# Optimization experiments

Hardware: AMD Instinct MI355X
Metric: run time of the kernel (lower is better)

Reference implementation:

```python
import jax, jax.numpy as jnp
import numpy as np

B, P, ENC = 64, 49, 1280
T, V, E, H, A = 25, 10000, 512, 1024, 512


def setup_inputs() -> dict:
    key = jax.random.key(0)
    ks = jax.random.split(key, 20)
    s = 0.02
    return {
        "encoder_out": jax.random.normal(ks[0], (B, P, ENC), jnp.float32),
        "captions": jax.random.randint(ks[1], (B, T), 0, V, jnp.int32),
        "embed": jax.random.normal(ks[2], (V, E), jnp.float32) * s,
        "W_eatt": jax.random.normal(ks[3], (A, ENC), jnp.float32) * s,
        "b_eatt": jnp.zeros((A,), jnp.float32),
        "W_datt": jax.random.normal(ks[4], (A, H), jnp.float32) * s,
        "b_datt": jnp.zeros((A,), jnp.float32),
        "W_fatt": jax.random.normal(ks[5], (1, A), jnp.float32) * s,
        "b_fatt": jnp.zeros((1,), jnp.float32),
        "W_ih": jax.random.normal(ks[6], (4 * H, E + ENC), jnp.float32) * s,
        "b_ih": jnp.zeros((4 * H,), jnp.float32),
        "W_hh": jax.random.normal(ks[7], (4 * H, H), jnp.float32) * s,
        "b_hh": jnp.zeros((4 * H,), jnp.float32),
        "W_h0": jax.random.normal(ks[8], (H, ENC), jnp.float32) * s,
        "b_h0": jnp.zeros((H,), jnp.float32),
        "W_c0": jax.random.normal(ks[9], (H, ENC), jnp.float32) * s,
        "b_c0": jnp.zeros((H,), jnp.float32),
        "W_out": jax.random.normal(ks[10], (V, H), jnp.float32) * s,
        "b_out": jnp.zeros((V,), jnp.float32),
    }


def reference(encoder_out, captions, embed, W_eatt, b_eatt, W_datt, b_datt,
              W_fatt, b_fatt, W_ih, b_ih, W_hh, b_hh, W_h0, b_h0, W_c0, b_c0,
              W_out, b_out):
    emb = embed[captions]                       # [B,T,E]
    mean_enc = encoder_out.mean(axis=1)         # [B,ENC]
    h0 = mean_enc @ W_h0.T + b_h0               # [B,H]
    c0 = mean_enc @ W_c0.T + b_c0
    # encoder-side attention projection is step-invariant; hoist out of loop
    att1 = encoder_out @ W_eatt.T + b_eatt      # [B,P,A]
    nH = h0.shape[-1]

    def step(carry, x_t):
        h, c = carry
        att2 = h @ W_datt.T + b_datt                          # [B,A]
        e = (jax.nn.relu(att1 + att2[:, None, :]) @ W_fatt.T + b_fatt)[..., 0]  # [B,P]
        alpha = jax.nn.softmax(e, axis=1)
        ctx = jnp.einsum('bp,bpe->be', alpha, encoder_out)    # [B,ENC]
        gin = jnp.concatenate([x_t, ctx], axis=1)             # [B,E+ENC]
        gates = gin @ W_ih.T + b_ih + h @ W_hh.T + b_hh       # [B,4H]
        i, f, g, o = jnp.split(gates, 4, axis=1)
        c_new = jax.nn.sigmoid(f) * c + jax.nn.sigmoid(i) * jnp.tanh(g)
        h_new = jax.nn.sigmoid(o) * jnp.tanh(c_new)
        preds = h_new @ W_out.T + b_out                       # dropout in eval mode = identity
        return (h_new, c_new), preds

    xs = jnp.swapaxes(emb[:, :-1, :], 0, 1)     # [T-1,B,E]
    _, preds = jax.lax.scan(step, (h0, c0), xs)
    return jnp.swapaxes(preds, 0, 1)            # [B,T-1,V]
```

## Files before the change

### kernel.cpp

```cpp
#include <hip/hip_runtime.h>
#include <hip/hip_bf16.h>

typedef float  v4f __attribute__((ext_vector_type(4)));
typedef short  v8s __attribute__((ext_vector_type(8)));
typedef int    v4i __attribute__((ext_vector_type(4)));

#define DEV static __device__ __forceinline__

DEV float bf2f(unsigned short u) {
    union { unsigned int i; float f; } x; x.i = ((unsigned int)u) << 16; return x.f;
}
DEV unsigned short f2bf(float f) {
    union { float f; unsigned int i; } x; x.f = f;
    unsigned int r = x.i + 0x7fff + ((x.i >> 16) & 1);
    return (unsigned short)(r >> 16);
}
DEV float sigm(float x) { return 1.f / (1.f + __expf(-x)); }

DEV v4i pack8(const float* f) {
    v4i o;
#pragma unroll
    for (int q = 0; q < 4; ++q)
        ((unsigned int*)&o)[q] = (unsigned int)f2bf(f[2 * q]) |
                                 ((unsigned int)f2bf(f[2 * q + 1]) << 16);
    return o;
}
DEV float lo16(unsigned int x) { union { unsigned int i; float f; } u; u.i = x << 16; return u.f; }
DEV float hi16(unsigned int x) { union { unsigned int i; float f; } u; u.i = x & 0xffff0000u; return u.f; }

__global__ __launch_bounds__(256) void uber_init(
    const float* __restrict__ Wih, const float* __restrict__ Whh,
    const float* __restrict__ bih, const float* __restrict__ bhh,
    const float* __restrict__ WoutF, const float* __restrict__ WeattF,
    const float* __restrict__ WdattF, const float* __restrict__ Wh0F,
    const float* __restrict__ Wc0F, const float* __restrict__ enc,
    const int* __restrict__ caps, const float* __restrict__ embed,
    unsigned short* __restrict__ Wz, unsigned short* __restrict__ Woutb,
    unsigned short* __restrict__ Weattb, unsigned short* __restrict__ Wdattb,
    unsigned short* __restrict__ Wh0b, unsigned short* __restrict__ Wc0b,
    unsigned short* __restrict__ encb, unsigned short* __restrict__ embb,
    unsigned short* __restrict__ meanb, float* __restrict__ bz)
{
    const int i = (blockIdx.x * 256 + threadIdx.x) * 8;
    float f[8];
    if (i < 11534336) {
        int n = i / 2816, k = i - n * 2816;
        const float* src = (k < 1792) ? &Wih[n * 1792 + k] : &Whh[n * 1024 + (k - 1792)];
        *(v4f*)&f[0] = *(const v4f*)src; *(v4f*)&f[4] = *(const v4f*)(src + 4);
        *(v4i*)&Wz[i] = pack8(f);
    } else if (i < 21774336) {
        int j = i - 11534336;
        *(v4f*)&f[0] = *(const v4f*)&WoutF[j]; *(v4f*)&f[4] = *(const v4f*)&WoutF[j + 4];
        *(v4i*)&Woutb[j] = pack8(f);
    } else if (i < 22429696) {
        int j = i - 21774336;
        *(v4f*)&f[0] = *(const v4f*)&WeattF[j]; *(v4f*)&f[4] = *(const v4f*)&WeattF[j + 4];
        *(v4i*)&Weattb[j] = pack8(f);
    } else if (i < 22953984) {
        int j = i - 22429696;
        *(v4f*)&f[0] = *(const v4f*)&WdattF[j]; *(v4f*)&f[4] = *(const v4f*)&WdattF[j + 4];
        *(v4i*)&Wdattb[j] = pack8(f);
    } else if (i < 24264704) {
        int j = i - 22953984;
        *(v4f*)&f[0] = *(const v4f*)&Wh0F[j]; *(v4f*)&f[4] = *(const v4f*)&Wh0F[j + 4];
        *(v4i*)&Wh0b[j] = pack8(f);
    } else if (i < 25575424) {
        int j = i - 24264704;
        *(v4f*)&f[0] = *(const v4f*)&Wc0F[j]; *(v4f*)&f[4] = *(const v4f*)&Wc0F[j + 4];
        *(v4i*)&Wc0b[j] = pack8(f);
    } else if (i < 29589504) {
        int j = i - 25575424;
        *(v4f*)&f[0] = *(const v4f*)&enc[j]; *(v4f*)&f[4] = *(const v4f*)&enc[j + 4];
        *(v4i*)&encb[j] = pack8(f);
    } else if (i < 30375936) {
        int j = i - 29589504;
        int b = j / 12288, r = j - b * 12288, t = r / 512, e = r - t * 512;
        const float* src = &embed[caps[b * 25 + t] * 512 + e];
        *(v4f*)&f[0] = *(const v4f*)src; *(v4f*)&f[4] = *(const v4f*)(src + 4);
        *(v4i*)&embb[j] = pack8(f);
    } else if (i < 30457856) {
        int j = i - 30375936;
        int b = j / 1280, c = j - b * 1280;
#pragma unroll
        for (int q = 0; q < 8; ++q) f[q] = 0.f;
        for (int p = 0; p < 49; ++p) {
            const float* src = &enc[(b * 49 + p) * 1280 + c];
            v4f a = *(const v4f*)src, bq = *(const v4f*)(src + 4);
#pragma unroll
            for (int q = 0; q < 4; ++q) { f[q] += a[q]; f[q + 4] += bq[q]; }
        }
#pragma unroll
        for (int q = 0; q < 8; ++q) f[q] *= (1.f / 49.f);
        *(v4i*)&meanb[j] = pack8(f);
    } else if (i < 30461952) {
        int j = i - 30457856;
#pragma unroll
        for (int q = 0; q < 8; ++q) f[q] = bih[j + q] + bhh[j + q];
        *(v4f*)&bz[j] = *(v4f*)&f[0]; *(v4f*)&bz[j + 4] = *(v4f*)&f[4];
    }
}

template <int OUT_BF16>
__global__ __launch_bounds__(256) void gemm64_bn16(
    const unsigned short* __restrict__ Ag, int lda,
    const unsigned short* __restrict__ Bg, int K,
    const float* __restrict__ bias, void* __restrict__ Cg, int ldc)
{
    __shared__ unsigned short lA[64 * 264];
    __shared__ unsigned short lB[16 * 264];
    const int tid = threadIdx.x, lane = tid & 63, w = tid >> 6;
    const int nb = blockIdx.x * 16;
    const int rA = tid >> 5, cA = (tid & 31) * 8;
    v4f acc = {0.f, 0.f, 0.f, 0.f};
    v4i ra[8], rb[2];
#pragma unroll
    for (int i = 0; i < 8; ++i)
        ra[i] = *(const v4i*)&Ag[(rA + i * 8) * lda + cA];
#pragma unroll
    for (int i = 0; i < 2; ++i)
        rb[i] = *(const v4i*)&Bg[(nb + rA + i * 8) * K + cA];
    for (int kt = 0; kt < K; kt += 256) {
#pragma unroll
        for (int i = 0; i < 8; ++i) *(v4i*)&lA[(rA + i * 8) * 264 + cA] = ra[i];
#pragma unroll
        for (int i = 0; i < 2; ++i) *(v4i*)&lB[(rA + i * 8) * 264 + cA] = rb[i];
        __syncthreads();
        if (kt + 256 < K) {
#pragma unroll
            for (int i = 0; i < 8; ++i)
                ra[i] = *(const v4i*)&Ag[(rA + i * 8) * lda + kt + 256 + cA];
#pragma unroll
            for (int i = 0; i < 2; ++i)
                rb[i] = *(const v4i*)&Bg[(nb + rA + i * 8) * K + kt + 256 + cA];
        }
#pragma unroll
        for (int ks = 0; ks < 8; ++ks) {
            v8s a = *(const v8s*)&lA[(w * 16 + (lane & 15)) * 264 + ks * 32 + (lane >> 4) * 8];
            v8s b = *(const v8s*)&lB[(lane & 15) * 264 + ks * 32 + (lane >> 4) * 8];
            acc = __builtin_amdgcn_mfma_f32_16x16x32_bf16(a, b, acc, 0, 0, 0);
        }
        __syncthreads();
    }
    const int n = nb + (lane & 15);
    const float bs = bias[n];
#pragma unroll
    for (int r = 0; r < 4; ++r) {
        int m = w * 16 + (lane >> 4) * 4 + r;
        float v = acc[r] + bs;
        if (OUT_BF16) ((unsigned short*)Cg)[m * ldc + n] = f2bf(v);
        else          ((float*)Cg)[m * ldc + n] = v;
    }
}

__global__ __launch_bounds__(256) void gemm_att1_k(
    const unsigned short* __restrict__ Aenc, const unsigned short* __restrict__ Bw,
    const float* __restrict__ bias, unsigned short* __restrict__ Cout)
{
    __shared__ unsigned short lA[64 * 136];
    __shared__ unsigned short lB[64 * 136];
    const int tid = threadIdx.x, lane = tid & 63, w = tid >> 6;
    const int mb = blockIdx.y * 64, nb = blockIdx.x * 64;
    const int rT = tid >> 4, cT = (tid & 15) * 8;
    v4f acc[4];
#pragma unroll
    for (int f = 0; f < 4; ++f) acc[f] = (v4f){0.f, 0.f, 0.f, 0.f};
    v4i ra[4], rb[4];
#pragma unroll
    for (int i = 0; i < 4; ++i) {
        ra[i] = *(const v4i*)&Aenc[(mb + rT + i * 16) * 1280 + cT];
        rb[i] = *(const v4i*)&Bw[(nb + rT + i * 16) * 1280 + cT];
    }
    for (int kt = 0; kt < 1280; kt += 128) {
#pragma unroll
        for (int i = 0; i < 4; ++i) {
            *(v4i*)&lA[(rT + i * 16) * 136 + cT] = ra[i];
            *(v4i*)&lB[(rT + i * 16) * 136 + cT] = rb[i];
        }
        __syncthreads();
        if (kt + 128 < 1280) {
#pragma unroll
            for (int i = 0; i < 4; ++i) {
                ra[i] = *(const v4i*)&Aenc[(mb + rT + i * 16) * 1280 + kt + 128 + cT];
                rb[i] = *(const v4i*)&Bw[(nb + rT + i * 16) * 1280 + kt + 128 + cT];
            }
        }
#pragma unroll
        for (int ks = 0; ks < 4; ++ks) {
            v8s a = *(const v8s*)&lA[(w * 16 + (lane & 15)) * 136 + ks * 32 + (lane >> 4) * 8];
#pragma unroll
            for (int f = 0; f < 4; ++f) {
                v8s b = *(const v8s*)&lB[(f * 16 + (lane & 15)) * 136 + ks * 32 + (lane >> 4) * 8];
                acc[f] = __builtin_amdgcn_mfma_f32_16x16x32_bf16(a, b, acc[f], 0, 0, 0);
            }
        }
        __syncthreads();
    }
#pragma unroll
    for (int f = 0; f < 4; ++f) {
        int n = nb + f * 16 + (lane & 15);
        float bs = bias[n];
#pragma unroll
        for (int r = 0; r < 4; ++r) {
            int m = mb + w * 16 + (lane >> 4) * 4 + r;
            Cout[m * 512 + n] = f2bf(acc[f][r] + bs);
        }
    }
}

__global__ __launch_bounds__(256) void attn_ctx_k(
    const float* __restrict__ att2, const unsigned short* __restrict__ att1b,
    const float* __restrict__ Wfatt, const float* __restrict__ bfatt,
    const unsigned short* __restrict__ encb, const unsigned short* __restrict__ embb,
    unsigned short* __restrict__ z, int tstep)
{
    __shared__ float a2[512];
    __shared__ float wf[512];
    __shared__ float es[64];
    __shared__ float alpha[64];
    const int tid = threadIdx.x, lane = tid & 63, w = tid >> 6;
    const int b = blockIdx.x;
    a2[tid]       = att2[b * 512 + tid];
    a2[tid + 256] = att2[b * 512 + tid + 256];
    wf[tid]       = Wfatt[tid];
    wf[tid + 256] = Wfatt[tid + 256];
    __syncthreads();
    for (int p = w; p < 49; p += 4) {
        v4i u = *(const v4i*)&att1b[(b * 49 + p) * 512 + lane * 8];
        v4f c0 = *(const v4f*)&a2[lane * 8], c1 = *(const v4f*)&a2[lane * 8 + 4];
        v4f w0 = *(const v4f*)&wf[lane * 8], w1 = *(const v4f*)&wf[lane * 8 + 4];
        float s = 0.f;
#pragma unroll
        for (int q = 0; q < 4; ++q) {
            unsigned int x = ((unsigned int*)&u)[q];
            float vlo = lo16(x), vhi = hi16(x);
            float clo = (q < 2) ? c0[q * 2] : c1[q * 2 - 4];
            float chi = (q < 2) ? c0[q * 2 + 1] : c1[q * 2 - 3];
            float wlo = (q < 2) ? w0[q * 2] : w1[q * 2 - 4];
            float whi = (q < 2) ? w0[q * 2 + 1] : w1[q * 2 - 3];
            s += fmaxf(vlo + clo, 0.f) * wlo;
            s += fmaxf(vhi + chi, 0.f) * whi;
        }
#pragma unroll
        for (int off = 32; off > 0; off >>= 1) s += __shfl_xor(s, off);
        if (lane == 0) es[p] = s + bfatt[0];
    }
    __syncthreads();
    if (w == 0) {
        float v = (lane < 49) ? es[lane] : -1e30f;
        float m = v;
#pragma unroll
        for (int off = 32; off > 0; off >>= 1) m = fmaxf(m, __shfl_xor(m, off));
        float e = (lane < 49) ? __expf(v - m) : 0.f;
        float s = e;
#pragma unroll
        for (int off = 32; off > 0; off >>= 1) s += __shfl_xor(s, off);
        if (lane < 49) alpha[lane] = e / s;
    }
    __syncthreads();
    if (tid < 160) {
        const int jb = tid * 8;
        float acc[8];
#pragma unroll
        for (int q = 0; q < 8; ++q) acc[q] = 0.f;
        for (int p = 0; p < 49; ++p) {
            v4i u = *(const v4i*)&encb[(b * 49 + p) * 1280 + jb];
            float al = alpha[p];
#pragma unroll
            for (int q = 0; q < 4; ++q) {
                unsigned int x = ((unsigned int*)&u)[q];
                acc[2 * q]     += al * lo16(x);
                acc[2 * q + 1] += al * hi16(x);
            }
        }
        *(v4i*)&z[b * 2816 + 512 + jb] = pack8(acc);
    }
    if (tid < 64)
        *(v4i*)&z[b * 2816 + tid * 8] = *(const v4i*)&embb[(b * 24 + tstep) * 512 + tid * 8];
}

__global__ __launch_bounds__(256) void gates_lstm_k(
    const unsigned short* __restrict__ z, const unsigned short* __restrict__ Wz,
    const float* __restrict__ bz, float* __restrict__ cst,
    unsigned short* __restrict__ zh, unsigned short* __restrict__ HallT)
{
    __shared__ unsigned short lA[64 * 264];
    __shared__ unsigned short lB[16 * 264];
    __shared__ float gbuf[64 * 20];
    const int tid = threadIdx.x, lane = tid & 63, w = tid >> 6;
    const int hb = blockIdx.x * 4;
    const int rT = tid >> 5, cT = (tid & 31) * 8;
    const int gate = rT & 3, hco = rT >> 2;
    const int growB = (gate * 1024 + hb + hco) * 2816;
    const int growB2 = (((rT + 8) & 3) * 1024 + hb + ((rT + 8) >> 2)) * 2816;
    v4f acc = {0.f, 0.f, 0.f, 0.f};
    v4i ra[8], rb[2];
#pragma unroll
    for (int i = 0; i < 8; ++i)
        ra[i] = *(const v4i*)&z[(rT + i * 8) * 2816 + cT];
    rb[0] = *(const v4i*)&Wz[growB + cT];
    rb[1] = *(const v4i*)&Wz[growB2 + cT];
    for (int kt = 0; kt < 2816; kt += 256) {
#pragma unroll
        for (int i = 0; i < 8; ++i) *(v4i*)&lA[(rT + i * 8) * 264 + cT] = ra[i];
        *(v4i*)&lB[rT * 264 + cT] = rb[0];
        *(v4i*)&lB[(rT + 8) * 264 + cT] = rb[1];
        __syncthreads();
        if (kt + 256 < 2816) {
#pragma unroll
            for (int i = 0; i < 8; ++i)
                ra[i] = *(const v4i*)&z[(rT + i * 8) * 2816 + kt + 256 + cT];
            rb[0] = *(const v4i*)&Wz[growB + kt + 256 + cT];
            rb[1] = *(const v4i*)&Wz[growB2 + kt + 256 + cT];
        }
#pragma unroll
        for (int ks = 0; ks < 8; ++ks) {
            v8s a = *(const v8s*)&lA[(w * 16 + (lane & 15)) * 264 + ks * 32 + (lane >> 4) * 8];
            v8s b = *(const v8s*)&lB[(lane & 15) * 264 + ks * 32 + (lane >> 4) * 8];
            acc = __builtin_amdgcn_mfma_f32_16x16x32_bf16(a, b, acc, 0, 0, 0);
        }
        __syncthreads();
    }
#pragma unroll
    for (int r = 0; r < 4; ++r) {
        int m = w * 16 + (lane >> 4) * 4 + r;
        int n = lane & 15;
        gbuf[m * 20 + n] = acc[r];
    }
    __syncthreads();
    const int b = tid >> 2, hc2 = tid & 3, hidx = hb + hc2;
    float gi = gbuf[b * 20 + hc2 * 4 + 0] + bz[hidx];
    float gf = gbuf[b * 20 + hc2 * 4 + 1] + bz[1024 + hidx];
    float gg = gbuf[b * 20 + hc2 * 4 + 2] + bz[2048 + hidx];
    float go = gbuf[b * 20 + hc2 * 4 + 3] + bz[3072 + hidx];
    float cn = sigm(gf) * cst[b * 1024 + hidx] + sigm(gi) * tanhf(gg);
    float hn = sigm(go) * tanhf(cn);
    cst[b * 1024 + hidx] = cn;
    unsigned short hb16 = f2bf(hn);
    zh[b * 2816 + hidx] = hb16;
    HallT[b * 1024 + hidx] = hb16;
}

__global__ __launch_bounds__(256) void preds_k(
    const unsigned short* __restrict__ Hall, const unsigned short* __restrict__ Wout,
    const float* __restrict__ bout, float* __restrict__ out)
{
    __shared__ unsigned short lA[128 * 72];
    __shared__ unsigned short lB[128 * 72];
    const int tid = threadIdx.x, lane = tid & 63, w = tid >> 6;
    const int mb = blockIdx.y * 128, nb = blockIdx.x * 128;
    const int rT = tid >> 3, cT = (tid & 7) * 8;
    int nB = nb + rT; if (nB > 9999) nB = 9999;
    v4f acc[2][8];
#pragma unroll
    for (int i = 0; i < 2; ++i)
#pragma unroll
        for (int f = 0; f < 8; ++f) acc[i][f] = (v4f){0.f, 0.f, 0.f, 0.f};
    v4i ra[4], rb[4];
#pragma unroll
    for (int i = 0; i < 4; ++i) {
        ra[i] = *(const v4i*)&Hall[(mb + rT + i * 32) * 1024 + cT];
        int n2 = nb + rT + i * 32; if (n2 > 9999) n2 = 9999;
        rb[i] = *(const v4i*)&Wout[n2 * 1024 + cT];
    }
    for (int kt = 0; kt < 1024; kt += 64) {
#pragma unroll
        for (int i = 0; i < 4; ++i) {
            *(v4i*)&lA[(rT + i * 32) * 72 + cT] = ra[i];
            *(v4i*)&lB[(rT + i * 32) * 72 + cT] = rb[i];
        }
        __syncthreads();
        if (kt + 64 < 1024) {
#pragma unroll
            for (int i = 0; i < 4; ++i) {
                ra[i] = *(const v4i*)&Hall[(mb + rT + i * 32) * 1024 + kt + 64 + cT];
                int n2 = nb + rT + i * 32; if (n2 > 9999) n2 = 9999;
                rb[i] = *(const v4i*)&Wout[n2 * 1024 + kt + 64 + cT];
            }
        }
#pragma unroll
        for (int ks = 0; ks < 2; ++ks) {
            int ko = ks * 32 + (lane >> 4) * 8;
            v8s a0 = *(const v8s*)&lA[(w * 32 + (lane & 15)) * 72 + ko];
            v8s a1 = *(const v8s*)&lA[(w * 32 + 16 + (lane & 15)) * 72 + ko];
#pragma unroll
            for (int f = 0; f < 8; ++f) {
                v8s b = *(const v8s*)&lB[(f * 16 + (lane & 15)) * 72 + ko];
                acc[0][f] = __builtin_amdgcn_mfma_f32_16x16x32_bf16(a0, b, acc[0][f], 0, 0, 0);
                acc[1][f] = __builtin_amdgcn_mfma_f32_16x16x32_bf16(a1, b, acc[1][f], 0, 0, 0);
            }
        }
        __syncthreads();
    }
#pragma unroll
    for (int f = 0; f < 8; ++f) {
        int n = nb + f * 16 + (lane & 15);
        if (n < 10000) {
            float bs = bout[n];
#pragma unroll
            for (int i = 0; i < 2; ++i)
#pragma unroll
                for (int r = 0; r < 4; ++r) {
                    int m = mb + w * 32 + i * 16 + (lane >> 4) * 4 + r;
                    int tt = m >> 6, bb = m & 63;
                    out[(bb * 24 + tt) * 10000 + n] = acc[i][f][r] + bs;
                }
        }
    }
}

extern "C" void kernel_launch(void* const* d_in, const int* in_sizes, int n_in,
                              void* d_out, int out_size, void* d_ws, size_t ws_size,
                              hipStream_t stream)
{
    const float* enc   = (const float*)d_in[0];
    const int*   caps  = (const int*)d_in[1];
    const float* embed = (const float*)d_in[2];
    const float* Weatt = (const float*)d_in[3];
    const float* beatt = (const float*)d_in[4];
    const float* Wdatt = (const float*)d_in[5];
    const float* bdatt = (const float*)d_in[6];
    const float* Wfatt = (const float*)d_in[7];
    const float* bfatt = (const float*)d_in[8];
    const float* Wih   = (const float*)d_in[9];
    const float* bih   = (const float*)d_in[10];
    const float* Whh   = (const float*)d_in[11];
    const float* bhh   = (const float*)d_in[12];
    const float* Wh0   = (const float*)d_in[13];
    const float* bh0   = (const float*)d_in[14];
    const float* Wc0   = (const float*)d_in[15];
    const float* bc0   = (const float*)d_in[16];
    const float* WoutF = (const float*)d_in[17];
    const float* bout  = (const float*)d_in[18];
    float* out = (float*)d_out;

    char* ws = (char*)d_ws;
    size_t off = 0;
    auto carve = [&](size_t bytes) -> void* {
        void* p = ws + off; off += (bytes + 255) & ~(size_t)255; return p;
    };
    unsigned short* Wzb    = (unsigned short*)carve(11534336ull * 2);
    unsigned short* Woutb  = (unsigned short*)carve(10240000ull * 2);
    unsigned short* Weattb = (unsigned short*)carve(655360ull * 2);
    unsigned short* Wdattb = (unsigned short*)carve(524288ull * 2);
    unsigned short* Wh0b   = (unsigned short*)carve(1310720ull * 2);
    unsigned short* Wc0b   = (unsigned short*)carve(1310720ull * 2);
    unsigned short* encb   = (unsigned short*)carve(4014080ull * 2);
    unsigned short* embb   = (unsigned short*)carve(786432ull * 2);
    unsigned short* meanb  = (unsigned short*)carve(81920ull * 2);
    unsigned short* att1b  = (unsigned short*)carve(1605632ull * 2);
    unsigned short* Hallb  = (unsigned short*)carve(1572864ull * 2);
    unsigned short* zb     = (unsigned short*)carve(180224ull * 2);
    float* bz   = (float*)carve(4096ull * 4);
    float* att2 = (float*)carve(32768ull * 4);
    float* cst  = (float*)carve(65536ull * 4);

    uber_init<<<14874, 256, 0, stream>>>(Wih, Whh, bih, bhh, WoutF, Weatt, Wdatt,
        Wh0, Wc0, enc, caps, embed, Wzb, Woutb, Weattb, Wdattb, Wh0b, Wc0b,
        encb, embb, meanb, bz);

    gemm64_bn16<1><<<64, 256, 0, stream>>>(meanb, 1280, Wh0b, 1280, bh0, zb + 1792, 2816);
    gemm64_bn16<0><<<64, 256, 0, stream>>>(meanb, 1280, Wc0b, 1280, bc0, cst, 1024);

    gemm_att1_k<<<dim3(8, 49), 256, 0, stream>>>(encb, Weattb, beatt, att1b);

    for (int t = 0; t < 24; ++t) {
        gemm64_bn16<0><<<32, 256, 0, stream>>>(zb + 1792, 2816, Wdattb, 1024, bdatt, att2, 512);
        attn_ctx_k<<<64, 256, 0, stream>>>(att2, att1b, Wfatt, bfatt, encb, embb, zb, t);
        gates_lstm_k<<<256, 256, 0, stream>>>(zb, Wzb, bz, cst, zb + 1792,
                                              Hallb + (size_t)t * 64 * 1024);
    }

    preds_k<<<dim3(79, 12), 256, 0, stream>>>(Hallb, Woutb, bout, out);
}
```

Baseline: 1.133 ms.

## Fuse recurrent loop into persistent kernel with global atomic barriers

Replaces the 72 per-timestep kernel launches (att2 GEMM, attention/context, gates+LSTM) with one persistent 256-block kernel that runs all 24 steps, separating the phases with a software grid barrier built on an atomic counter. The hidden state moves to a separate hnew buffer that is copied into z during the attention phase. The output projection kernel also gets a 1D grid with an XCD-aware block-to-tile mapping to improve L2 locality. This removes launch overhead and inter-kernel gaps, but it depends on all 256 blocks being co-resident and adds barrier spin cost.

Result: slower. 4.130 ms (+264.4%).

```diff
diff --git a/kernel.cpp b/kernel.cpp
--- a/kernel.cpp
+++ b/kernel.cpp
@@ -27,6 +27,18 @@
 }
 DEV float lo16(unsigned int x) { union { unsigned int i; float f; } u; u.i = x << 16; return u.f; }
 DEV float hi16(unsigned int x) { union { unsigned int i; float f; } u; u.i = x & 0xffff0000u; return u.f; }
+
+DEV void gbar(int* cnt, int target) {
+    __syncthreads();
+    if (threadIdx.x == 0) {
+        __threadfence();
+        __hip_atomic_fetch_add(cnt, 1, __ATOMIC_RELEASE, __HIP_MEMORY_SCOPE_AGENT);
+        while (__hip_atomic_load(cnt, __ATOMIC_ACQUIRE, __HIP_MEMORY_SCOPE_AGENT) < target)
+            __builtin_amdgcn_s_sleep(2);
+        __threadfence();
+    }
+    __syncthreads();
+}
 
 __global__ __launch_bounds__(256) void uber_init(
     const float* __restrict__ Wih, const float* __restrict__ Whh,
@@ -207,149 +219,215 @@
     }
 }
 
-__global__ __launch_bounds__(256) void attn_ctx_k(
-    const float* __restrict__ att2, const unsigned short* __restrict__ att1b,
-    const float* __restrict__ Wfatt, const float* __restrict__ bfatt,
-    const unsigned short* __restrict__ encb, const unsigned short* __restrict__ embb,
-    unsigned short* __restrict__ z, int tstep)
+struct SmemGemm {
+    unsigned short lA[64 * 264];
+    unsigned short lB[16 * 264];
+    float gbuf[64 * 20];
+};
+struct SmemAttn {
+    float a2[512];
+    float wf[512];
+    float es[64];
+    float alpha[64];
+};
+union LoopSmem { SmemGemm g; SmemAttn a; };
+
+__global__ __launch_bounds__(256, 1) void loop_k(
+    float* __restrict__ att2, unsigned short* __restrict__ zb,
+    const unsigned short* __restrict__ Wdattb, const float* __restrict__ bdatt,
+    const unsigned short* __restrict__ att1b, const float* __restrict__ Wfatt,
+    const float* __restrict__ bfatt, const unsigned short* __restrict__ encb,
+    const unsigned short* __restrict__ embb, const unsigned short* __restrict__ Wzb,
+    const float* __restrict__ bz, float* __restrict__ cst,
+    unsigned short* __restrict__ Hallb, unsigned short* __restrict__ hnewb,
+    int* __restrict__ barcnt)
 {
-    __shared__ float a2[512];
-    __shared__ float wf[512];
-    __shared__ float es[64];
-    __shared__ float alpha[64];
+    __shared__ LoopSmem sm;
     const int tid = threadIdx.x, lane = tid & 63, w = tid >> 6;
-    const int b = blockIdx.x;
-    a2[tid]       = att2[b * 512 + tid];
-    a2[tid + 256] = att2[b * 512 + tid + 256];
-    wf[tid]       = Wfatt[tid];
-    wf[tid + 256] = Wfatt[tid + 256];
-    __syncthreads();
-    for (int p = w; p < 49; p += 4) {
-        v4i u = *(const v4i*)&att1b[(b * 49 + p) * 512 + lane * 8];
-        v4f c0 = *(const v4f*)&a2[lane * 8], c1 = *(const v4f*)&a2[lane * 8 + 4];
-        v4f w0 = *(const v4f*)&wf[lane * 8], w1 = *(const v4f*)&wf[lane * 8 + 4];
-        float s = 0.f;
-#pragma unroll
-        for (int q = 0; q < 4; ++q) {
-            unsigned int x = ((unsigned int*)&u)[q];
-            float vlo = lo16(x), vhi = hi16(x);
-            float clo = (q < 2) ? c0[q * 2] : c1[q * 2 - 4];
-            float chi = (q < 2) ? c0[q * 2 + 1] : c1[q * 2 - 3];
-            float wlo = (q < 2) ? w0[q * 2] : w1[q * 2 - 4];
-            float whi = (q < 2) ? w0[q * 2 + 1] : w1[q * 2 - 3];
-            s += fmaxf(vlo + clo, 0.f) * wlo;
-            s += fmaxf(vhi + chi, 0.f) * whi;
-        }
-#pragma unroll
-        for (int off = 32; off > 0; off >>= 1) s += __shfl_xor(s, off);
-        if (lane == 0) es[p] = s + bfatt[0];
-    }
-    __syncthreads();
-    if (w == 0) {
-        float v = (lane < 49) ? es[lane] : -1e30f;
-        float m = v;
-#pragma unroll
-        for (int off = 32; off > 0; off >>= 1) m = fmaxf(m, __shfl_xor(m, off));
-        float e = (lane < 49) ? __expf(v - m) : 0.f;
-        float s = e;
-#pragma unroll
-        for (int off = 32; off > 0; off >>= 1) s += __shfl_xor(s, off);
-        if (lane < 49) alpha[lane] = e / s;
-    }
-    __syncthreads();
-    if (tid < 160) {
-        const int jb = tid * 8;
-        float acc[8];
-#pragma unroll
-        for (int q = 0; q < 8; ++q) acc[q] = 0.f;
-        for (int p = 0; p < 49; ++p) {
-            v4i u = *(const v4i*)&encb[(b * 49 + p) * 1280 + jb];
-            float al = alpha[p];
-#pragma unroll
-            for (int q = 0; q < 4; ++q) {
-                unsigned int x = ((unsigned int*)&u)[q];
-                acc[2 * q]     += al * lo16(x);
-                acc[2 * q + 1] += al * hi16(x);
-            }
-        }
-        *(v4i*)&z[b * 2816 + 512 + jb] = pack8(acc);
-    }
-    if (tid < 64)
-        *(v4i*)&z[b * 2816 + tid * 8] = *(const v4i*)&embb[(b * 24 + tstep) * 512 + tid * 8];
-}
-
-__global__ __launch_bounds__(256) void gates_lstm_k(
-    const unsigned short* __restrict__ z, const unsigned short* __restrict__ Wz,
-    const float* __restrict__ bz, float* __restrict__ cst,
-    unsigned short* __restrict__ zh, unsigned short* __restrict__ HallT)
-{
-    __shared__ unsigned short lA[64 * 264];
-    __shared__ unsigned short lB[16 * 264];
-    __shared__ float gbuf[64 * 20];
-    const int tid = threadIdx.x, lane = tid & 63, w = tid >> 6;
-    const int hb = blockIdx.x * 4;
-    const int rT = tid >> 5, cT = (tid & 31) * 8;
-    const int gate = rT & 3, hco = rT >> 2;
-    const int growB = (gate * 1024 + hb + hco) * 2816;
-    const int growB2 = (((rT + 8) & 3) * 1024 + hb + ((rT + 8) >> 2)) * 2816;
-    v4f acc = {0.f, 0.f, 0.f, 0.f};
-    v4i ra[8], rb[2];
-#pragma unroll
-    for (int i = 0; i < 8; ++i)
-        ra[i] = *(const v4i*)&z[(rT + i * 8) * 2816 + cT];
-    rb[0] = *(const v4i*)&Wz[growB + cT];
-    rb[1] = *(const v4i*)&Wz[growB2 + cT];
-    for (int kt = 0; kt < 2816; kt += 256) {
-#pragma unroll
-        for (int i = 0; i < 8; ++i) *(v4i*)&lA[(rT + i * 8) * 264 + cT] = ra[i];
-        *(v4i*)&lB[rT * 264 + cT] = rb[0];
-        *(v4i*)&lB[(rT + 8) * 264 + cT] = rb[1];
-        __syncthreads();
-        if (kt + 256 < 2816) {
+    const int bid = blockIdx.x;
+    int btarget = 0;
+
+    for (int t = 0; t < 24; ++t) {
+        if (bid < 32) {
+            const int nb = bid * 16;
+            const int rA = tid >> 5, cA = (tid & 31) * 8;
+            v4f acc = {0.f, 0.f, 0.f, 0.f};
+            v4i ra[8], rb[2];
 #pragma unroll
             for (int i = 0; i < 8; ++i)
-                ra[i] = *(const v4i*)&z[(rT + i * 8) * 2816 + kt + 256 + cT];
-            rb[0] = *(const v4i*)&Wz[growB + kt + 256 + cT];
-            rb[1] = *(const v4i*)&Wz[growB2 + kt + 256 + cT];
-        }
-#pragma unroll
-        for (int ks = 0; ks < 8; ++ks) {
-            v8s a = *(const v8s*)&lA[(w * 16 + (lane & 15)) * 264 + ks * 32 + (lane >> 4) * 8];
-            v8s b = *(const v8s*)&lB[(lane & 15) * 264 + ks * 32 + (lane >> 4) * 8];
-            acc = __builtin_amdgcn_mfma_f32_16x16x32_bf16(a, b, acc, 0, 0, 0);
-        }
-        __syncthreads();
-    }
-#pragma unroll
-    for (int r = 0; r < 4; ++r) {
-        int m = w * 16 + (lane >> 4) * 4 + r;
-        int n = lane & 15;
-        gbuf[m * 20 + n] = acc[r];
-    }
-    __syncthreads();
-    const int b = tid >> 2, hc2 = tid & 3, hidx = hb + hc2;
-    float gi = gbuf[b * 20 + hc2 * 4 + 0] + bz[hidx];
-    float gf = gbuf[b * 20 + hc2 * 4 + 1] + bz[1024 + hidx];
-    float gg = gbuf[b * 20 + hc2 * 4 + 2] + bz[2048 + hidx];
-    float go = gbuf[b * 20 + hc2 * 4 + 3] + bz[3072 + hidx];
-    float cn = sigm(gf) * cst[b * 1024 + hidx] + sigm(gi) * tanhf(gg);
-    float hn = sigm(go) * tanhf(cn);
-    cst[b * 1024 + hidx] = cn;
-    unsigned short hb16 = f2bf(hn);
-    zh[b * 2816 + hidx] = hb16;
-    HallT[b * 1024 + hidx] = hb16;
+                ra[i] = *(const v4i*)&hnewb[(rA + i * 8) * 1024 + cA];
+#pragma unroll
+            for (int i = 0; i < 2; ++i)
+                rb[i] = *(const v4i*)&Wdattb[(nb + rA + i * 8) * 1024 + cA];
+            for (int kt = 0; kt < 1024; kt += 256) {
+#pragma unroll
+                for (int i = 0; i < 8; ++i) *(v4i*)&sm.g.lA[(rA + i * 8) * 264 + cA] = ra[i];
+#pragma unroll
+                for (int i = 0; i < 2; ++i) *(v4i*)&sm.g.lB[(rA + i * 8) * 264 + cA] = rb[i];
+                __syncthreads();
+                if (kt + 256 < 1024) {
+#pragma unroll
+                    for (int i = 0; i < 8; ++i)
+                        ra[i] = *(const v4i*)&hnewb[(rA + i * 8) * 1024 + kt + 256 + cA];
+#pragma unroll
+                    for (int i = 0; i < 2; ++i)
+                        rb[i] = *(const v4i*)&Wdattb[(nb + rA + i * 8) * 1024 + kt + 256 + cA];
+                }
+#pragma unroll
+                for (int ks = 0; ks < 8; ++ks) {
+                    v8s a = *(const v8s*)&sm.g.lA[(w * 16 + (lane & 15)) * 264 + ks * 32 + (lane >> 4) * 8];
+                    v8s b = *(const v8s*)&sm.g.lB[(lane & 15) * 264 + ks * 32 + (lane >> 4) * 8];
+                    acc = __builtin_amdgcn_mfma_f32_16x16x32_bf16(a, b, acc, 0, 0, 0);
+                }
+                __syncthreads();
+            }
+            const int n = nb + (lane & 15);
+            const float bs = bdatt[n];
+#pragma unroll
+            for (int r = 0; r < 4; ++r) {
+                int m = w * 16 + (lane >> 4) * 4 + r;
+                att2[m * 512 + n] = acc[r] + bs;
+            }
+        }
+        btarget += 256; gbar(barcnt, btarget);
+
+        if (bid < 64) {
+            const int b = bid;
+            float* a2 = sm.a.a2; float* wf = sm.a.wf;
+            float* es = sm.a.es; float* alpha = sm.a.alpha;
+            a2[tid]       = att2[b * 512 + tid];
+            a2[tid + 256] = att2[b * 512 + tid + 256];
+            wf[tid]       = Wfatt[tid];
+            wf[tid + 256] = Wfatt[tid + 256];
+            __syncthreads();
+            for (int p = w; p < 49; p += 4) {
+                v4i u = *(const v4i*)&att1b[(b * 49 + p) * 512 + lane * 8];
+                v4f c0 = *(const v4f*)&a2[lane * 8], c1 = *(const v4f*)&a2[lane * 8 + 4];
+                v4f w0 = *(const v4f*)&wf[lane * 8], w1 = *(const v4f*)&wf[lane * 8 + 4];
+                float s = 0.f;
+#pragma unroll
+                for (int q = 0; q < 4; ++q) {
+                    unsigned int x = ((unsigned int*)&u)[q];
+                    float vlo = lo16(x), vhi = hi16(x);
+                    float clo = (q < 2) ? c0[q * 2] : c1[q * 2 - 4];
+                    float chi = (q < 2) ? c0[q * 2 + 1] : c1[q * 2 - 3];
+                    float wlo = (q < 2) ? w0[q * 2] : w1[q * 2 - 4];
+                    float whi = (q < 2) ? w0[q * 2 + 1] : w1[q * 2 - 3];
+                    s += fmaxf(vlo + clo, 0.f) * wlo;
+                    s += fmaxf(vhi + chi, 0.f) * whi;
+                }
+#pragma unroll
+                for (int off = 32; off > 0; off >>= 1) s += __shfl_xor(s, off);
+                if (lane == 0) es[p] = s + bfatt[0];
+            }
+            __syncthreads();
+            if (w == 0) {
+                float v = (lane < 49) ? es[lane] : -1e30f;
+                float m = v;
+#pragma unroll
+                for (int off = 32; off > 0; off >>= 1) m = fmaxf(m, __shfl_xor(m, off));
+                float e = (lane < 49) ? __expf(v - m) : 0.f;
+                float s = e;
+#pragma unroll
+                for (int off = 32; off > 0; off >>= 1) s += __shfl_xor(s, off);
+                if (lane < 49) alpha[lane] = e / s;
+            }
+            __syncthreads();
+            if (tid < 160) {
+                const int jb = tid * 8;
+                float acc[8];
+#pragma unroll
+                for (int q = 0; q < 8; ++q) acc[q] = 0.f;
+                for (int p = 0; p < 49; ++p) {
+                    v4i u = *(const v4i*)&encb[(b * 49 + p) * 1280 + jb];
+                    float al = alpha[p];
+#pragma unroll
+                    for (int q = 0; q < 4; ++q) {
+                        unsigned int x = ((unsigned int*)&u)[q];
+                        acc[2 * q]     += al * lo16(x);
+                        acc[2 * q + 1] += al * hi16(x);
+                    }
+                }
+                *(v4i*)&zb[b * 2816 + 512 + jb] = pack8(acc);
+            }
+            if (tid < 64)
+                *(v4i*)&zb[b * 2816 + tid * 8] = *(const v4i*)&embb[(b * 24 + t) * 512 + tid * 8];
+            if (tid < 128)
+                *(v4i*)&zb[b * 2816 + 1792 + tid * 8] = *(const v4i*)&hnewb[b * 1024 + tid * 8];
+        }
+        btarget += 256; gbar(barcnt, btarget);
+
+        {
+            const int hb = bid * 4;
+            const int rT = tid >> 5, cT = (tid & 31) * 8;
+            const int gate = rT & 3, hco = rT >> 2;
+            const int growB  = (gate * 1024 + hb + hco) * 2816;
+            const int growB2 = (((rT + 8) & 3) * 1024 + hb + ((rT + 8) >> 2)) * 2816;
+            v4f acc = {0.f, 0.f, 0.f, 0.f};
+            v4i ra[8], rb[2];
+#pragma unroll
+            for (int i = 0; i < 8; ++i)
+                ra[i] = *(const v4i*)&zb[(rT + i * 8) * 2816 + cT];
+            rb[0] = *(const v4i*)&Wzb[growB + cT];
+            rb[1] = *(const v4i*)&Wzb[growB2 + cT];
+            for (int kt = 0; kt < 2816; kt += 256) {
+#pragma unroll
+                for (int i = 0; i < 8; ++i) *(v4i*)&sm.g.lA[(rT + i * 8) * 264 + cT] = ra[i];
+                *(v4i*)&sm.g.lB[rT * 264 + cT] = rb[0];
+                *(v4i*)&sm.g.lB[(rT + 8) * 264 + cT] = rb[1];
+                __syncthreads();
+                if (kt + 256 < 2816) {
+#pragma unroll
+                    for (int i = 0; i < 8; ++i)
+                        ra[i] = *(const v4i*)&zb[(rT + i * 8) * 2816 + kt + 256 + cT];
+                    rb[0] = *(const v4i*)&Wzb[growB + kt + 256 + cT];
+                    rb[1] = *(const v4i*)&Wzb[growB2 + kt + 256 + cT];
+                }
+#pragma unroll
+                for (int ks = 0; ks < 8; ++ks) {
+                    v8s a = *(const v8s*)&sm.g.lA[(w * 16 + (lane & 15)) * 264 + ks * 32 + (lane >> 4) * 8];
+                    v8s b = *(const v8s*)&sm.g.lB[(lane & 15) * 264 + ks * 32 + (lane >> 4) * 8];
+                    acc = __builtin_amdgcn_mfma_f32_16x16x32_bf16(a, b, acc, 0, 0, 0);
+                }
+                __syncthreads();
+            }
+#pragma unroll
+            for (int r = 0; r < 4; ++r) {
+                int m = w * 16 + (lane >> 4) * 4 + r;
+                int n = lane & 15;
+                sm.g.gbuf[m * 20 + n] = acc[r];
+            }
+            __syncthreads();
+            const int b = tid >> 2, hc2 = tid & 3, hidx = hb + hc2;
+            float gi = sm.g.gbuf[b * 20 + hc2 * 4 + 0] + bz[hidx];
+            float gf = sm.g.gbuf[b * 20 + hc2 * 4 + 1] + bz[1024 + hidx];
+            float gg = sm.g.gbuf[b * 20 + hc2 * 4 + 2] + bz[2048 + hidx];
+            float go = sm.g.gbuf[b * 20 + hc2 * 4 + 3] + bz[3072 + hidx];
+            float cn = sigm(gf) * cst[b * 1024 + hidx] + sigm(gi) * tanhf(gg);
+            float hn = sigm(go) * tanhf(cn);
+            cst[b * 1024 + hidx] = cn;
+            unsigned short h16 = f2bf(hn);
+            hnewb[b * 1024 + hidx] = h16;
+            Hallb[(size_t)t * 65536 + b * 1024 + hidx] = h16;
+        }
+        if (t < 23) { btarget += 256; gbar(barcnt, btarget); }
+    }
 }
 
 __global__ __launch_bounds__(256) void preds_k(
     const unsigned short* __restrict__ Hall, const unsigned short* __restrict__ Wout,
     const float* __restrict__ bout, float* __restrict__ out)
 {
+    const int bidl = blockIdx.x;
+    const int xcd = bidl & 7, loc = bidl >> 3;
+    const int nbi = xcd * 10 + loc / 12;
+    const int mbi = loc - (loc / 12) * 12;
+    if (nbi >= 79) return;
     __shared__ unsigned short lA[128 * 72];
     __shared__ unsigned short lB[128 * 72];
     const int tid = threadIdx.x, lane = tid & 63, w = tid >> 6;
-    const int mb = blockIdx.y * 128, nb = blockIdx.x * 128;
+    const int mb = mbi * 128, nb = nbi * 128;
     const int rT = tid >> 3, cT = (tid & 7) * 8;
-    int nB = nb + rT; if (nB > 9999) nB = 9999;
     v4f acc[2][8];
 #pragma unroll
     for (int i = 0; i < 2; ++i)
@@ -450,25 +528,25 @@
     unsigned short* att1b  = (unsigned short*)carve(1605632ull * 2);
     unsigned short* Hallb  = (unsigned short*)carve(1572864ull * 2);
     unsigned short* zb     = (unsigned short*)carve(180224ull * 2);
+    unsigned short* hnewb  = (unsigned short*)carve(65536ull * 2);
     float* bz   = (float*)carve(4096ull * 4);
     float* att2 = (float*)carve(32768ull * 4);
     float* cst  = (float*)carve(65536ull * 4);
+    int*   barcnt = (int*)carve(256);
+
+    hipMemsetAsync(barcnt, 0, 256, stream);
 
     uber_init<<<14874, 256, 0, stream>>>(Wih, Whh, bih, bhh, WoutF, Weatt, Wdatt,
         Wh0, Wc0, enc, caps, embed, Wzb, Woutb, Weattb, Wdattb, Wh0b, Wc0b,
         encb, embb, meanb, bz);
 
-    gemm64_bn16<1><<<64, 256, 0, stream>>>(meanb, 1280, Wh0b, 1280, bh0, zb + 1792, 2816);
+    gemm64_bn16<1><<<64, 256, 0, stream>>>(meanb, 1280, Wh0b, 1280, bh0, hnewb, 1024);
     gemm64_bn16<0><<<64, 256, 0, stream>>>(meanb, 1280, Wc0b, 1280, bc0, cst, 1024);
 
     gemm_att1_k<<<dim3(8, 49), 256, 0, stream>>>(encb, Weattb, beatt, att1b);
 
-    for (int t = 0; t < 24; ++t) {
-        gemm64_bn16<0><<<32, 256, 0, stream>>>(zb + 1792, 2816, Wdattb, 1024, bdatt, att2, 512);
-        attn_ctx_k<<<64, 256, 0, stream>>>(att2, att1b, Wfatt, bfatt, encb, embb, zb, t);
-        gates_lstm_k<<<256, 256, 0, stream>>>(zb, Wzb, bz, cst, zb + 1792,
-                                              Hallb + (size_t)t * 64 * 1024);
-    }
-
-    preds_k<<<dim3(79, 12), 256, 0, stream>>>(Hallb, Woutb, bout, out);
-}
+    loop_k<<<256, 256, 0, stream>>>(att2, zb, Wdattb, bdatt, att1b, Wfatt,
+        bfatt, encb, embb, Wzb, bz, cst, Hallb, hnewb, barcnt);
+
+    preds_k<<<960, 256, 0, stream>>>(Hallb, Woutb, bout, out);
+}
```
